# Optimization experiments

Hardware: AMD Instinct MI355X
Metric: run time of the kernel (lower is better)

Reference implementation:

```python
import jax, jax.numpy as jnp
from jax import lax
import numpy as np

B = 32        # graphs per batch
NN = 513      # nodes per graph (odd M so Y/Z head lengths match)
IN = 128      # input_dim
OUT = 256     # output_dim
T = 4         # edge_types
STEPS = 4     # ggnn propagation steps
DEG = 16
N = B * NN
E = N * DEG
CAT = IN + OUT


def setup_inputs() -> dict:
    key = jax.random.key(0)
    ks = jax.random.split(key, 16)
    f32 = jnp.float32
    feature = jax.random.normal(ks[0], (N, IN), f32)
    offs = (jnp.arange(B) * NN)[:, None]
    edge_src = (jax.random.randint(ks[1], (B, NN * DEG), 0, NN) + offs).reshape(-1)
    edge_dst = (jax.random.randint(ks[2], (B, NN * DEG), 0, NN) + offs).reshape(-1)
    edge_type = jax.random.randint(ks[3], (E,), 0, T)
    s = 1.0 / np.sqrt(OUT)
    W_msg = jax.random.normal(ks[4], (T, OUT, OUT), f32) * s      # [T, out, in] (torch Linear layout)
    b_msg = jnp.zeros((T, OUT), f32)
    gru_w_ih = jax.random.normal(ks[5], (3 * OUT, OUT), f32) * s
    gru_w_hh = jax.random.normal(ks[6], (3 * OUT, OUT), f32) * s
    gru_b_ih = jnp.zeros((3 * OUT,), f32)
    gru_b_hh = jnp.zeros((3 * OUT,), f32)
    conv1_w = jax.random.normal(ks[7], (OUT, OUT, 3), f32) * (1.0 / np.sqrt(OUT * 3))
    conv1_b = jnp.zeros((OUT,), f32)
    conv2_w = jax.random.normal(ks[8], (OUT, OUT, 1), f32) * s
    conv2_b = jnp.zeros((OUT,), f32)
    convc1_w = jax.random.normal(ks[9], (CAT, CAT, 3), f32) * (1.0 / np.sqrt(CAT * 3))
    convc1_b = jnp.zeros((CAT,), f32)
    convc2_w = jax.random.normal(ks[10], (CAT, CAT, 2), f32) * (1.0 / np.sqrt(CAT * 2))
    convc2_b = jnp.zeros((CAT,), f32)
    mlpy_w = jax.random.normal(ks[11], (1, OUT), f32) * s
    mlpy_b = jnp.zeros((1,), f32)
    mlpz_w = jax.random.normal(ks[12], (1, CAT), f32) * (1.0 / np.sqrt(CAT))
    mlpz_b = jnp.zeros((1,), f32)
    return dict(feature=feature, W_msg=W_msg, b_msg=b_msg,
                gru_w_ih=gru_w_ih, gru_w_hh=gru_w_hh, gru_b_ih=gru_b_ih, gru_b_hh=gru_b_hh,
                conv1_w=conv1_w, conv1_b=conv1_b, conv2_w=conv2_w, conv2_b=conv2_b,
                convc1_w=convc1_w, convc1_b=convc1_b, convc2_w=convc2_w, convc2_b=convc2_b,
                mlpy_w=mlpy_w, mlpy_b=mlpy_b, mlpz_w=mlpz_w, mlpz_b=mlpz_b,
                edge_src=edge_src, edge_dst=edge_dst, edge_type=edge_type)


def _conv1d(x, w, b):
    # x: [B, C_in, L], w: [C_out, C_in, K]
    y = lax.conv_general_dilated(x, w, (1,), 'VALID', dimension_numbers=('NCH', 'OIH', 'NCH'))
    return y + b[None, :, None]


def _maxpool1d(x, k, s):
    init = jnp.array(-jnp.inf, dtype=x.dtype)
    return lax.reduce_window(x, init, lax.max, (1, 1, k), (1, 1, s), 'VALID')


def _forward(feature, W_msg, b_msg, gru_w_ih, gru_w_hh, gru_b_ih, gru_b_hh,
             conv1_w, conv1_b, conv2_w, conv2_b, convc1_w, convc1_b, convc2_w, convc2_b,
             mlpy_w, mlpy_b, mlpz_w, mlpz_b, edge_src, edge_dst, edge_type):
    # --- GatedGraphConv (DGL semantics): zero-pad features to out_feats ---
    h = jnp.pad(feature, ((0, 0), (0, OUT - IN)))  # [N, OUT]
    for _ in range(STEPS):
        # per-etype linear on all nodes: hw[t] = h @ W_msg[t].T + b_msg[t]
        hw = jnp.einsum('nd,tod->tno', h, W_msg) + b_msg[:, None, :]   # [T, N, OUT]
        msg = hw[edge_type, edge_src]                                   # [E, OUT] gather
        a = jax.ops.segment_sum(msg, edge_dst, num_segments=N)          # [N, OUT] scatter-add
        # GRUCell(a, h) in torch gate order (r, z, n)
        gi = a @ gru_w_ih.T + gru_b_ih
        gh = h @ gru_w_hh.T + gru_b_hh
        ir, iz, inn = jnp.split(gi, 3, axis=-1)
        hr, hz, hn = jnp.split(gh, 3, axis=-1)
        r = jax.nn.sigmoid(ir + hr)
        z = jax.nn.sigmoid(iz + hz)
        n = jnp.tanh(inn + r * hn)
        h = (1.0 - z) * n + z * h
    outputs = h                                             # [N, OUT]
    ci = jnp.concatenate([outputs, feature], axis=-1)       # [N, OUT+IN]
    # batchify to [B, C, L]
    hi = outputs.reshape(B, NN, OUT).transpose(0, 2, 1)
    cb = ci.reshape(B, NN, CAT).transpose(0, 2, 1)
    Y1 = _maxpool1d(jax.nn.relu(_conv1d(hi, conv1_w, conv1_b)), 3, 2)
    Y2 = _maxpool1d(jax.nn.relu(_conv1d(Y1, conv2_w, conv2_b)), 2, 2).transpose(0, 2, 1)   # [B, 127, OUT]
    Z1 = _maxpool1d(jax.nn.relu(_conv1d(cb, convc1_w, convc1_b)), 3, 2)
    Z2 = _maxpool1d(jax.nn.relu(_conv1d(Z1, convc2_w, convc2_b)), 2, 2).transpose(0, 2, 1)  # [B, 127, CAT]
    before_avg = (Y2 @ mlpy_w.T + mlpy_b) * (Z2 @ mlpz_w.T + mlpz_b)   # [B, 127, 1]
    avg = before_avg.mean(axis=1)                                       # [B, 1]
    return jax.nn.sigmoid(avg).squeeze(-1)                              # [B]


def reference(feature, W_msg, b_msg, gru_w_ih, gru_w_hh, gru_b_ih, gru_b_hh,
              conv1_w, conv1_b, conv2_w, conv2_b, convc1_w, convc1_b, convc2_w, convc2_b,
              mlpy_w, mlpy_b, mlpz_w, mlpz_b, edge_src, edge_dst, edge_type):
    return _forward(feature, W_msg, b_msg, gru_w_ih, gru_w_hh, gru_b_ih, gru_b_hh,
                    conv1_w, conv1_b, conv2_w, conv2_b, convc1_w, convc1_b, convc2_w, convc2_b,
                    mlpy_w, mlpy_b, mlpz_w, mlpz_b, edge_src, edge_dst, edge_type)
```

## Files before the change

### kernel.cpp

```cpp
#include <hip/hip_runtime.h>

#define Bg    32
#define NNg   513
#define INF   128
#define OUTF  256
#define TT    4
#define NSTEP 4
#define DEGg  16
#define Ntot  (Bg*NNg)
#define Etot  (Ntot*DEGg)
#define CATF  (OUTF+INF)
#define SK    1056
#define NB    (Ntot*TT)
#define NSB2  129

typedef _Float16 h8_t __attribute__((ext_vector_type(8)));
typedef _Float16 h4_t __attribute__((ext_vector_type(4)));
typedef float    f4_t __attribute__((ext_vector_type(4)));

#define GLL(gsrc, ldst)                                                        \
  __builtin_amdgcn_global_load_lds(                                            \
      (const __attribute__((address_space(1))) unsigned int*)(gsrc),           \
      (__attribute__((address_space(3))) unsigned int*)(ldst), 16, 0, 0)

__global__ void pad_h_k(const float* __restrict__ feat, float* __restrict__ h,
                        _Float16* __restrict__ h16) {
  int idx = blockIdx.x*256 + threadIdx.x;
  if (idx >= Ntot*OUTF) return;
  int n = idx >> 8, c = idx & 255;
  float v = (c < INF) ? feat[n*INF + c] : 0.f;
  h[idx] = v;
  h16[idx] = (_Float16)v;
}

__global__ void cvt_k(const float* __restrict__ s, _Float16* __restrict__ d, int n) {
  int i = (blockIdx.x*256 + threadIdx.x) * 4;
  if (i >= n) return;
  float4 v = *reinterpret_cast<const float4*>(s + i);
  _Float16 o[4] = {(_Float16)v.x, (_Float16)v.y, (_Float16)v.z, (_Float16)v.w};
  *reinterpret_cast<ushort4*>(d + i) = *reinterpret_cast<ushort4*>(o);
}

__global__ void build_cb16_k(const _Float16* __restrict__ h16,
                             const float* __restrict__ feat,
                             _Float16* __restrict__ cb) {
  int idx = blockIdx.x*256 + threadIdx.x;
  if (idx >= Ntot*CATF) return;
  int n = idx / CATF, c = idx % CATF;
  cb[idx] = (c < OUTF) ? h16[n*OUTF + c] : (_Float16)feat[n*INF + (c - OUTF)];
}

__global__ void zero_int_k(int* __restrict__ p, int n) {
  int i = blockIdx.x*256 + threadIdx.x;
  if (i < n) p[i] = 0;
}

__global__ void hist_k(const int* __restrict__ dst, const int* __restrict__ typ,
                       int* __restrict__ cnt) {
  int e = blockIdx.x*256 + threadIdx.x;
  if (e < Etot) atomicAdd(&cnt[dst[e]*TT + typ[e]], 1);
}

__global__ void scan1_k(const int* __restrict__ cnt, int* __restrict__ rp2,
                        int* __restrict__ bsum) {
  __shared__ int buf[512];
  int t = threadIdx.x;
  int i = blockIdx.x*512 + t;
  int v = (i < NB) ? cnt[i] : 0;
  buf[t] = v;
  __syncthreads();
  #pragma unroll
  for (int off = 1; off < 512; off <<= 1) {
    int x = (t >= off) ? buf[t - off] : 0;
    __syncthreads();
    buf[t] += x;
    __syncthreads();
  }
  if (i < NB) rp2[i] = buf[t] - v;
  if (t == 511) bsum[blockIdx.x] = buf[511];
}

__global__ void scan2_k(int* __restrict__ bsum) {
  __shared__ int buf[256];
  int t = threadIdx.x;
  int v = (t < NSB2) ? bsum[t] : 0;
  buf[t] = v;
  __syncthreads();
  #pragma unroll
  for (int off = 1; off < 256; off <<= 1) {
    int x = (t >= off) ? buf[t - off] : 0;
    __syncthreads();
    buf[t] += x;
    __syncthreads();
  }
  if (t < NSB2) bsum[t] = buf[t] - v;
}

__global__ void scan3_k(int* __restrict__ rp2, const int* __restrict__ bsum) {
  int i = blockIdx.x*512 + threadIdx.x;
  if (i < NB) rp2[i] += bsum[blockIdx.x];
  if (i == 0) rp2[NB] = Etot;
}

__global__ void fill_k(const int* __restrict__ dst, const int* __restrict__ typ,
                       const int* __restrict__ src, const int* __restrict__ rp2,
                       int* __restrict__ cursor, int* __restrict__ srcv) {
  int e = blockIdx.x*256 + threadIdx.x;
  if (e < Etot) {
    int b = dst[e]*TT + typ[e];
    int pos = atomicAdd(&cursor[b], 1);
    srcv[rp2[b] + pos] = src[e];
  }
}

__global__ void gather_k(const _Float16* __restrict__ h16, const int* __restrict__ rp2,
                         const int* __restrict__ srcv, _Float16* __restrict__ s16) {
  __shared__ int src_s[128];
  int n = blockIdx.x;
  int c = threadIdx.x;
  int b0 = rp2[TT*n], e1 = rp2[TT*n+1], e2 = rp2[TT*n+2], e3 = rp2[TT*n+3], e4 = rp2[TT*n+4];
  float a0 = 0.f, a1 = 0.f, a2 = 0.f, a3 = 0.f;
  for (int base = b0; base < e4; base += 128) {
    int m = e4 - base; if (m > 128) m = 128;
    if (c < m) src_s[c] = srcv[base + c];
    __syncthreads();
    int s1 = min(max(e1 - base, 0), m);
    int s2 = min(max(e2 - base, 0), m);
    int s3 = min(max(e3 - base, 0), m);
#define SEG(ACC, ST, EN)                                                   \
    {                                                                      \
      int i = (ST);                                                        \
      for (; i + 4 <= (EN); i += 4) {                                      \
        float v0 = (float)h16[(size_t)src_s[i]  *256 + c];                 \
        float v1 = (float)h16[(size_t)src_s[i+1]*256 + c];                 \
        float v2 = (float)h16[(size_t)src_s[i+2]*256 + c];                 \
        float v3 = (float)h16[(size_t)src_s[i+3]*256 + c];                 \
        ACC += (v0 + v1) + (v2 + v3);                                      \
      }                                                                    \
      for (; i < (EN); ++i) ACC += (float)h16[(size_t)src_s[i]*256 + c];   \
    }
    SEG(a0, 0,  s1)
    SEG(a1, s1, s2)
    SEG(a2, s2, s3)
    SEG(a3, s3, m)
#undef SEG
    __syncthreads();
  }
  size_t b = (size_t)n * SK;
  s16[b + 0*256 + c] = (_Float16)a0;
  s16[b + 1*256 + c] = (_Float16)a1;
  s16[b + 2*256 + c] = (_Float16)a2;
  s16[b + 3*256 + c] = (_Float16)a3;
  if (c < 32) {
    int cv = (c == 0) ? (e1-b0) : (c == 1) ? (e2-e1) : (c == 2) ? (e3-e2) : (c == 3) ? (e4-e3) : 0;
    s16[b + 1024 + c] = (_Float16)(float)cv;
  }
}

__global__ void repack_wext_k(const float* __restrict__ Wmsg, const float* __restrict__ bmsg,
                              _Float16* __restrict__ wext) {
  int idx = blockIdx.x*256 + threadIdx.x;
  if (idx >= 256*SK) return;
  int co = idx / SK, k = idx % SK;
  float v;
  if (k < 1024)      { int t = k >> 8, ci = k & 255; v = Wmsg[((size_t)t*256 + co)*256 + ci]; }
  else if (k < 1028) { v = bmsg[(k - 1024)*256 + co]; }
  else               { v = 0.f; }
  wext[idx] = (_Float16)v;
}

__global__ void gru_gate_k(const _Float16* __restrict__ gi, const _Float16* __restrict__ gh,
                           float* __restrict__ h, _Float16* __restrict__ h16) {
  int idx = blockIdx.x*256 + threadIdx.x;
  if (idx >= Ntot*64) return;
  int n = idx >> 6, g4 = (idx & 63) * 4;
  const _Float16* gin = gi + (size_t)n*768 + g4;
  const _Float16* ghn = gh + (size_t)n*768 + g4;
  h4_t ir = *reinterpret_cast<const h4_t*>(gin);
  h4_t iz = *reinterpret_cast<const h4_t*>(gin + 256);
  h4_t in_ = *reinterpret_cast<const h4_t*>(gin + 512);
  h4_t hr = *reinterpret_cast<const h4_t*>(ghn);
  h4_t hz = *reinterpret_cast<const h4_t*>(ghn + 256);
  h4_t hn = *reinterpret_cast<const h4_t*>(ghn + 512);
  size_t hb = (size_t)n*256 + g4;
  float4 hv = *reinterpret_cast<const float4*>(h + hb);
  float hvv[4] = {hv.x, hv.y, hv.z, hv.w};
  float ov[4];
  _Float16 ov16[4];
  #pragma unroll
  for (int j = 0; j < 4; ++j) {
    float r  = 1.f / (1.f + expf(-((float)ir[j] + (float)hr[j])));
    float z  = 1.f / (1.f + expf(-((float)iz[j] + (float)hz[j])));
    float nn = tanhf((float)in_[j] + r * (float)hn[j]);
    float o = (1.f - z) * nn + z * hvv[j];
    ov[j] = o;
    ov16[j] = (_Float16)o;
  }
  float4 os = {ov[0], ov[1], ov[2], ov[3]};
  *reinterpret_cast<float4*>(h + hb) = os;
  *reinterpret_cast<ushort4*>(h16 + hb) = *reinterpret_cast<ushort4*>(ov16);
}

template<typename IT, typename OT>
__global__ void maxpool_k(const IT* __restrict__ in, OT* __restrict__ out,
                          int Lin, int Lp, int C, int kwin) {
  int idx = blockIdx.x*256 + threadIdx.x;
  int total = Bg*Lp*C;
  if (idx >= total) return;
  int c = idx % C; int r = idx / C; int p = r % Lp; int b = r / Lp;
  const IT* base = in + ((size_t)(b*Lin + 2*p))*C + c;
  float v = (float)base[0];
  for (int w = 1; w < kwin; ++w) v = fmaxf(v, (float)base[(size_t)w*C]);
  out[idx] = (OT)v;
}

__global__ void repack16_k(const float* __restrict__ w, _Float16* __restrict__ wk,
                           int Cout, int Cin, int K) {
  int idx = blockIdx.x*256 + threadIdx.x;
  int total = Cout*Cin*K;
  if (idx >= total) return;
  int ci = idx % Cin; int r = idx / Cin; int k = r % K; int co = r / K;
  wk[idx] = (_Float16)w[(co*Cin + ci)*K + k];
}

__global__ void head_k(const float* __restrict__ Y2, const float* __restrict__ Z2,
                       const float* __restrict__ wy, const float* __restrict__ by,
                       const float* __restrict__ wz, const float* __restrict__ bz,
                       float* __restrict__ out) {
  int b = blockIdx.x;
  int tid = threadIdx.x;
  __shared__ float red[128];
  float sum = 0.f;
  for (int p = tid; p < 127; p += 128) {
    const float* yr = Y2 + ((size_t)(b*127 + p))*OUTF;
    const float* zr = Z2 + ((size_t)(b*127 + p))*CATF;
    float yv = by[0], zv = bz[0];
    for (int c = 0; c < OUTF; ++c) yv = fmaf(yr[c], wy[c], yv);
    for (int c = 0; c < CATF; ++c) zv = fmaf(zr[c], wz[c], zv);
    sum += yv * zv;
  }
  red[tid] = sum;
  __syncthreads();
  for (int off = 64; off > 0; off >>= 1) {
    if (tid < off) red[tid] += red[tid + off];
    __syncthreads();
  }
  if (tid == 0) out[b] = 1.f / (1.f + expf(-red[0] / 127.f));
}

template<typename CT, bool RELU, bool MAPPED, bool DUAL>
__global__ __launch_bounds__(256, 3) void hgemm(
    const _Float16* __restrict__ A, const _Float16* __restrict__ W,
    const float* __restrict__ bias, CT* __restrict__ C,
    int M, int Nout, int K, int arstride, int Lout, int NNodes,
    const _Float16* A2, const _Float16* W2, const float* bias2, CT* C2) {
  __shared__ _Float16 As[128*32];
  __shared__ _Float16 Ws[128*32];
  if (DUAL && blockIdx.z == 1) { A = A2; W = W2; bias = bias2; C = C2; }
  int tid = threadIdx.x;
  int lane = tid & 63, wid = tid >> 6;
  int wm = wid >> 1, wn = wid & 1;
  int l15 = lane & 15, l4 = lane >> 4;
  int m0 = blockIdx.x * 128, n0 = blockIdx.y * 128;

  int sr  = wid*16 + (lane >> 2);
  int scol = ((lane & 3) ^ (sr & 3)) * 8;
  int am0r = m0 + sr, am1r = m0 + sr + 64;
  int am0 = (am0r < M) ? am0r : M - 1;
  int am1 = (am1r < M) ? am1r : M - 1;
  int an0 = MAPPED ? (am0 / Lout) * NNodes + (am0 % Lout) : am0;
  int an1 = MAPPED ? (am1 / Lout) * NNodes + (am1 % Lout) : am1;
  const _Float16* asrc0 = A + (size_t)an0 * arstride + scol;
  const _Float16* asrc1 = A + (size_t)an1 * arstride + scol;
  const _Float16* wsrc0 = W + (size_t)(n0 + sr) * K + scol;
  const _Float16* wsrc1 = W + (size_t)(n0 + sr + 64) * K + scol;
  _Float16* ald0 = As + (wid*16) * 32;
  _Float16* ald1 = As + (64 + wid*16) * 32;
  _Float16* wld0 = Ws + (wid*16) * 32;
  _Float16* wld1 = Ws + (64 + wid*16) * 32;

  int sl = l4 ^ (l15 & 3);
  f4_t acc[4][4] = {};

  for (int k0 = 0; k0 < K; k0 += 32) {
    if (k0) __syncthreads();
    GLL(asrc0 + k0, ald0);
    GLL(asrc1 + k0, ald1);
    GLL(wsrc0 + k0, wld0);
    GLL(wsrc1 + k0, wld1);
    __syncthreads();

    h8_t af[4], bf[4];
    #pragma unroll
    for (int fm = 0; fm < 4; ++fm)
      af[fm] = *reinterpret_cast<const h8_t*>(As + (wm*64 + fm*16 + l15)*32 + sl*8);
    #pragma unroll
    for (int fn = 0; fn < 4; ++fn)
      bf[fn] = *reinterpret_cast<const h8_t*>(Ws + (wn*64 + fn*16 + l15)*32 + sl*8);
    #pragma unroll
    for (int fm = 0; fm < 4; ++fm)
      #pragma unroll
      for (int fn = 0; fn < 4; ++fn)
        acc[fm][fn] = __builtin_amdgcn_mfma_f32_16x16x32_f16(af[fm], bf[fn], acc[fm][fn], 0, 0, 0);
  }

  #pragma unroll
  for (int fn = 0; fn < 4; ++fn) {
    int col = n0 + wn*64 + fn*16 + l15;
    float bv = bias[col];
    #pragma unroll
    for (int fm = 0; fm < 4; ++fm) {
      #pragma unroll
      for (int i = 0; i < 4; ++i) {
        int m = m0 + wm*64 + fm*16 + l4*4 + i;
        if (m >= M) continue;
        float v = acc[fm][fn][i] + bv;
        if (RELU) v = fmaxf(v, 0.f);
        C[(size_t)m * Nout + col] = (CT)v;
      }
    }
  }
}

static inline int cdiv(int x, int y) { return (x + y - 1) / y; }

extern "C" void kernel_launch(void* const* d_in, const int* in_sizes, int n_in,
                              void* d_out, int out_size, void* d_ws, size_t ws_size,
                              hipStream_t stream) {
  const float* feature  = (const float*)d_in[0];
  const float* W_msg    = (const float*)d_in[1];
  const float* b_msg    = (const float*)d_in[2];
  const float* w_ih     = (const float*)d_in[3];
  const float* w_hh     = (const float*)d_in[4];
  const float* b_ih     = (const float*)d_in[5];
  const float* b_hh     = (const float*)d_in[6];
  const float* conv1_w  = (const float*)d_in[7];
  const float* conv1_b  = (const float*)d_in[8];
  const float* conv2_w  = (const float*)d_in[9];
  const float* conv2_b  = (const float*)d_in[10];
  const float* convc1_w = (const float*)d_in[11];
  const float* convc1_b = (const float*)d_in[12];
  const float* convc2_w = (const float*)d_in[13];
  const float* convc2_b = (const float*)d_in[14];
  const float* mlpy_w   = (const float*)d_in[15];
  const float* mlpy_b   = (const float*)d_in[16];
  const float* mlpz_w   = (const float*)d_in[17];
  const float* mlpz_b   = (const float*)d_in[18];
  const int*   esrc     = (const int*)d_in[19];
  const int*   edst     = (const int*)d_in[20];
  const int*   etyp     = (const int*)d_in[21];
  float* out = (float*)d_out;

  char* base = (char*)d_ws;
  size_t off = 0;
  auto alloc = [&](size_t bytes) { void* p = base + off; off = (off + bytes + 255) & ~(size_t)255; return p; };
  float*    h      = (float*)   alloc((size_t)Ntot*OUTF*4);
  _Float16* h16    = (_Float16*)alloc((size_t)Ntot*OUTF*2);
  _Float16* Wext16 = (_Float16*)alloc((size_t)256*SK*2);
  _Float16* wih16  = (_Float16*)alloc((size_t)768*256*2);
  _Float16* whh16  = (_Float16*)alloc((size_t)768*256*2);
  float*    bias0  = (float*)   alloc(256*4);
  int* rp2    = (int*)alloc((NB+1)*4);
  int* cnt    = (int*)alloc(NB*4);
  int* bsum   = (int*)alloc(NSB2*4);
  int* srcv   = (int*)alloc((size_t)Etot*4);
  char* big   = (char*)alloc((size_t)Ntot*1536*4);
  _Float16* gi  = (_Float16*)big;
  _Float16* gh  = gi + (size_t)Ntot*768;
  _Float16* s16 = (_Float16*)(big + (size_t)Ntot*768*4);
  _Float16* a16 = s16 + (size_t)Ntot*SK;
  float*    Y2   = (float*)big;
  float*    Z2   = Y2 + (size_t)Bg*127*OUTF;
  _Float16* y1   = (_Float16*)(Z2 + (size_t)Bg*127*CATF);
  float*    y2   = (float*)(y1 + (size_t)Bg*511*OUTF);
  _Float16* p1   = (_Float16*)(y2 + (size_t)Bg*255*OUTF);
  _Float16* cb16 = p1 + (size_t)Bg*255*OUTF;
  _Float16* z1   = cb16 + (size_t)Ntot*CATF;
  float*    z2   = (float*)(z1 + (size_t)Bg*511*CATF);
  _Float16* pz1  = (_Float16*)(z2 + (size_t)Bg*254*CATF);
  _Float16* wk1  = pz1 + (size_t)Bg*255*CATF;
  _Float16* wkc1 = wk1 + (size_t)256*768;
  _Float16* wkc2 = wkc1 + (size_t)384*1152;
  _Float16* c2w16= wkc2 + (size_t)384*768;

  dim3 blk(256);

  pad_h_k<<<cdiv(Ntot*OUTF,256), blk, 0, stream>>>(feature, h, h16);
  repack_wext_k<<<cdiv(256*SK,256), blk, 0, stream>>>(W_msg, b_msg, Wext16);
  cvt_k<<<cdiv(768*256/4,256), blk, 0, stream>>>(w_ih, wih16, 768*256);
  cvt_k<<<cdiv(768*256/4,256), blk, 0, stream>>>(w_hh, whh16, 768*256);
  hipMemsetAsync(bias0, 0, 256*4, stream);

  zero_int_k<<<cdiv(NB,256), blk, 0, stream>>>(cnt, NB);
  hist_k<<<cdiv(Etot,256), blk, 0, stream>>>(edst, etyp, cnt);
  scan1_k<<<NSB2, 512, 0, stream>>>(cnt, rp2, bsum);
  scan2_k<<<1, blk, 0, stream>>>(bsum);
  scan3_k<<<NSB2, 512, 0, stream>>>(rp2, bsum);
  zero_int_k<<<cdiv(NB,256), blk, 0, stream>>>(cnt, NB);
  fill_k<<<cdiv(Etot,256), blk, 0, stream>>>(edst, etyp, esrc, rp2, cnt, srcv);

  for (int s = 0; s < NSTEP; ++s) {
    gather_k<<<Ntot, blk, 0, stream>>>(h16, rp2, srcv, s16);
    hgemm<_Float16,false,false,false><<<dim3(cdiv(Ntot,128), 2), blk, 0, stream>>>(
        s16, Wext16, bias0, a16, Ntot, 256, SK, SK, 0, 0,
        nullptr, nullptr, nullptr, nullptr);
    hgemm<_Float16,false,false,true><<<dim3(cdiv(Ntot,128), 6, 2), blk, 0, stream>>>(
        a16, wih16, b_ih, gi, Ntot, 768, 256, 256, 0, 0,
        h16, whh16, b_hh, gh);
    gru_gate_k<<<cdiv(Ntot*64,256), blk, 0, stream>>>(gi, gh, h, h16);
  }

  repack16_k<<<cdiv(256*256*3,256), blk, 0, stream>>>(conv1_w,  wk1,  256, 256, 3);
  repack16_k<<<cdiv(384*384*3,256), blk, 0, stream>>>(convc1_w, wkc1, 384, 384, 3);
  repack16_k<<<cdiv(384*384*2,256), blk, 0, stream>>>(convc2_w, wkc2, 384, 384, 2);
  cvt_k<<<cdiv(256*256/4,256), blk, 0, stream>>>(conv2_w, c2w16, 256*256);

  hgemm<_Float16,true,true,false><<<dim3(cdiv(Bg*511,128), 2), blk, 0, stream>>>(
      h16, wk1, conv1_b, y1, Bg*511, 256, 768, 256, 511, NNg,
      nullptr, nullptr, nullptr, nullptr);
  maxpool_k<_Float16,_Float16><<<cdiv(Bg*255*256,256), blk, 0, stream>>>(y1, p1, 511, 255, 256, 3);
  hgemm<float,true,false,false><<<dim3(cdiv(Bg*255,128), 2), blk, 0, stream>>>(
      p1, c2w16, conv2_b, y2, Bg*255, 256, 256, 256, 0, 0,
      nullptr, nullptr, nullptr, nullptr);
  maxpool_k<float,float><<<cdiv(Bg*127*256,256), blk, 0, stream>>>(y2, Y2, 255, 127, 256, 2);

  build_cb16_k<<<cdiv(Ntot*CATF,256), blk, 0, stream>>>(h16, feature, cb16);
  hgemm<_Float16,true,true,false><<<dim3(cdiv(Bg*511,128), 3), blk, 0, stream>>>(
      cb16, wkc1, convc1_b, z1, Bg*511, 384, 1152, 384, 511, NNg,
      nullptr, nullptr, nullptr, nullptr);
  maxpool_k<_Float16,_Float16><<<cdiv(Bg*255*384,256), blk, 0, stream>>>(z1, pz1, 511, 255, 384, 3);
  hgemm<float,true,true,false><<<dim3(cdiv(Bg*254,128), 3), blk, 0, stream>>>(
      pz1, wkc2, convc2_b, z2, Bg*254, 384, 768, 384, 254, 255,
      nullptr, nullptr, nullptr, nullptr);
  maxpool_k<float,float><<<cdiv(Bg*127*384,256), blk, 0, stream>>>(z2, Z2, 254, 127, 384, 2);

  head_k<<<Bg, 128, 0, stream>>>(Y2, Z2, mlpy_w, mlpy_b, mlpz_w, mlpz_b, out);
}
```

Measured before the change: 846.6 us.

## Double-buffer LDS tiles in hgemm and adjust swizzle and occupancy

```diff
diff --git a/kernel.cpp b/kernel.cpp
--- a/kernel.cpp
+++ b/kernel.cpp
@@ -249,13 +249,13 @@
 }
 
 template<typename CT, bool RELU, bool MAPPED, bool DUAL>
-__global__ __launch_bounds__(256, 3) void hgemm(
+__global__ __launch_bounds__(256, 4) void hgemm(
     const _Float16* __restrict__ A, const _Float16* __restrict__ W,
     const float* __restrict__ bias, CT* __restrict__ C,
     int M, int Nout, int K, int arstride, int Lout, int NNodes,
     const _Float16* A2, const _Float16* W2, const float* bias2, CT* C2) {
-  __shared__ _Float16 As[128*32];
-  __shared__ _Float16 Ws[128*32];
+  __shared__ _Float16 As[2][128*32];
+  __shared__ _Float16 Ws[2][128*32];
   if (DUAL && blockIdx.z == 1) { A = A2; W = W2; bias = bias2; C = C2; }
   int tid = threadIdx.x;
   int lane = tid & 63, wid = tid >> 6;
@@ -264,7 +264,7 @@
   int m0 = blockIdx.x * 128, n0 = blockIdx.y * 128;
 
   int sr  = wid*16 + (lane >> 2);
-  int scol = ((lane & 3) ^ (sr & 3)) * 8;
+  int scol = ((lane & 3) ^ ((sr >> 1) & 3)) * 8;
   int am0r = m0 + sr, am1r = m0 + sr + 64;
   int am0 = (am0r < M) ? am0r : M - 1;
   int am1 = (am1r < M) ? am1r : M - 1;
@@ -274,29 +274,35 @@
   const _Float16* asrc1 = A + (size_t)an1 * arstride + scol;
   const _Float16* wsrc0 = W + (size_t)(n0 + sr) * K + scol;
   const _Float16* wsrc1 = W + (size_t)(n0 + sr + 64) * K + scol;
-  _Float16* ald0 = As + (wid*16) * 32;
-  _Float16* ald1 = As + (64 + wid*16) * 32;
-  _Float16* wld0 = Ws + (wid*16) * 32;
-  _Float16* wld1 = Ws + (64 + wid*16) * 32;
-
-  int sl = l4 ^ (l15 & 3);
+  int ld0 = (wid*16) * 32;
+  int ld1 = (64 + wid*16) * 32;
+
+  int sl = l4 ^ ((l15 >> 1) & 3);
   f4_t acc[4][4] = {};
-
-  for (int k0 = 0; k0 < K; k0 += 32) {
-    if (k0) __syncthreads();
-    GLL(asrc0 + k0, ald0);
-    GLL(asrc1 + k0, ald1);
-    GLL(wsrc0 + k0, wld0);
-    GLL(wsrc1 + k0, wld1);
-    __syncthreads();
-
+  int T = K >> 5;
+
+  GLL(asrc0, &As[0][ld0]);
+  GLL(asrc1, &As[0][ld1]);
+  GLL(wsrc0, &Ws[0][ld0]);
+  GLL(wsrc1, &Ws[0][ld1]);
+
+  for (int t = 0; t < T; ++t) {
+    __syncthreads();
+    int cur = t & 1;
+    if (t + 1 < T) {
+      int k1 = (t + 1) << 5;
+      GLL(asrc0 + k1, &As[cur ^ 1][ld0]);
+      GLL(asrc1 + k1, &As[cur ^ 1][ld1]);
+      GLL(wsrc0 + k1, &Ws[cur ^ 1][ld0]);
+      GLL(wsrc1 + k1, &Ws[cur ^ 1][ld1]);
+    }
     h8_t af[4], bf[4];
     #pragma unroll
     for (int fm = 0; fm < 4; ++fm)
-      af[fm] = *reinterpret_cast<const h8_t*>(As + (wm*64 + fm*16 + l15)*32 + sl*8);
+      af[fm] = *reinterpret_cast<const h8_t*>(&As[cur][(wm*64 + fm*16 + l15)*32 + sl*8]);
     #pragma unroll
     for (int fn = 0; fn < 4; ++fn)
-      bf[fn] = *reinterpret_cast<const h8_t*>(Ws + (wn*64 + fn*16 + l15)*32 + sl*8);
+      bf[fn] = *reinterpret_cast<const h8_t*>(&Ws[cur][(wn*64 + fn*16 + l15)*32 + sl*8]);
     #pragma unroll
     for (int fm = 0; fm < 4; ++fm)
       #pragma unroll
```

After: 828.4 us. -2.1%, faster.
